# Performance work log

Hardware: AMD Instinct MI355X
Metric: run time of the kernel (lower is better)

## Reference

```python
import jax, jax.numpy as jnp
import numpy as np

D_MODEL = 512
NHEAD = 8
HEAD_DIM = D_MODEL // NHEAD
LN_EPS = 1e-5


def layer_norm(x, gamma, beta):
    mu = jnp.mean(x, axis=-1, keepdims=True)
    var = jnp.var(x, axis=-1, keepdims=True)
    return (x - mu) * jax.lax.rsqrt(var + LN_EPS) * gamma + beta


def setup_inputs() -> dict:
    key = jax.random.key(0)
    ks = jax.random.split(key, 10)
    B, L, S = 2, 4096, 4096
    d = D_MODEL
    s = 0.02
    return {
        "x": jax.random.normal(ks[0], (B, L, d), dtype=jnp.float32),
        "source": jax.random.normal(ks[1], (B, S, d), dtype=jnp.float32),
        "Wq": jax.random.normal(ks[2], (d, d), dtype=jnp.float32) * s,
        "Wk": jax.random.normal(ks[3], (d, d), dtype=jnp.float32) * s,
        "Wv": jax.random.normal(ks[4], (d, d), dtype=jnp.float32) * s,
        "Wm": jax.random.normal(ks[5], (d, d), dtype=jnp.float32) * s,
        "W1": jax.random.normal(ks[6], (2 * d, 2 * d), dtype=jnp.float32) * s,
        "W2": jax.random.normal(ks[7], (d, 2 * d), dtype=jnp.float32) * s,
        "g1": jnp.ones((d,), dtype=jnp.float32),
        "b1": jnp.zeros((d,), dtype=jnp.float32),
        "g2": jnp.ones((d,), dtype=jnp.float32),
        "b2": jnp.zeros((d,), dtype=jnp.float32),
    }


def reference(x, source, Wq, Wk, Wv, Wm, W1, W2, g1, b1, g2, b2):
    bs, L, _ = x.shape
    S = source.shape[1]
    # projections (torch Linear: y = x @ W^T), split into heads
    qw = (x @ Wq.T).reshape(bs, L, NHEAD, HEAD_DIM)
    kw = (source @ Wk.T).reshape(bs, S, NHEAD, HEAD_DIM)
    vw = (source @ Wv.T).reshape(bs, S, NHEAD, HEAD_DIM)
    # attention scores [B, L, S, H], softmax over S (axis=2)
    a = jnp.einsum('nlhd,nshd->nlsh', qw, kw) / jnp.sqrt(jnp.float32(HEAD_DIM))
    a = jax.nn.softmax(a, axis=2)
    o = jnp.einsum('nlsh,nshd->nlhd', a, vw).reshape(bs, L, NHEAD * HEAD_DIM)
    message = layer_norm(o @ Wm.T, g1, b1)
    h = jnp.concatenate([x, message], axis=2)  # [B, L, 2D]
    h = jax.nn.relu(h @ W1.T) @ W2.T
    message = layer_norm(h, g2, b2)
    return x + message
```

## Files before the change

### kernel.cpp

```cpp
#include <hip/hip_runtime.h>
#include <stdint.h>

typedef short bh8 __attribute__((ext_vector_type(8)));
typedef float fx4 __attribute__((ext_vector_type(4)));
typedef float fx16 __attribute__((ext_vector_type(16)));
typedef unsigned short u16;
typedef unsigned int u32;
typedef u32 u32x4 __attribute__((ext_vector_type(4)));
typedef u16 us4 __attribute__((ext_vector_type(4)));

#define NHEAD 8
#define HD 64
#define DM 512
#define SEQ 4096
#define ROWS 8192
#define CEXP 0.1803368801111244f

#define MODE_BF16 1
#define MODE_RELU_BF16 2
#define MODE_KV 3

__device__ __forceinline__ u16 f2bf(float f) {
  union { float f; u32 u; } x; x.f = f;
  u32 u = x.u;
  u = u + 0x7fffu + ((u >> 16) & 1u);
  return (u16)(u >> 16);
}
__device__ __forceinline__ float bf2f(u16 h) {
  union { u32 u; float f; } x; x.u = ((u32)h) << 16;
  return x.f;
}
__device__ __forceinline__ void gll16(const void* g, void* l) {
  __builtin_amdgcn_global_load_lds(
      (const __attribute__((address_space(1))) void*)(uintptr_t)g,
      (__attribute__((address_space(3))) void*)(uintptr_t)l,
      16, 0, 0);
}
__device__ __forceinline__ fx4 mfma16(bh8 a, bh8 b, fx4 c) {
  return __builtin_amdgcn_mfma_f32_16x16x32_bf16(a, b, c, 0, 0, 0);
}
__device__ __forceinline__ fx16 mfma32(bh8 a, bh8 b, fx16 c) {
  return __builtin_amdgcn_mfma_f32_32x32x16_bf16(a, b, c, 0, 0, 0);
}
__device__ __forceinline__ u32 cvtpk(float lo, float hi) {
  u32 r; asm("v_cvt_pk_bf16_f32 %0, %1, %2" : "=v"(r) : "v"(lo), "v"(hi));
  return r;
}
__device__ __forceinline__ void pswap(u32& a, u32& b) {
  auto r = __builtin_amdgcn_permlane32_swap(a, b, false, false);
  a = r[0]; b = r[1];
}

__device__ __forceinline__ int fragidx4(int n, int k4, int K) {
  return (((((n >> 4) * (K >> 5) + (k4 >> 5)) << 2) + ((k4 >> 3) & 3)) * 16 + (n & 15)) * 2
         + ((k4 & 7) >> 2);
}

__global__ __launch_bounds__(256) void cvt_all_kernel(
    const float* __restrict__ x, const float* __restrict__ src,
    const float* __restrict__ Wq, const float* __restrict__ Wk,
    const float* __restrict__ Wv, const float* __restrict__ Wm,
    const float* __restrict__ W1, const float* __restrict__ W2,
    u16* __restrict__ xb, u16* __restrict__ sb,
    u16* __restrict__ wqb, u16* __restrict__ wkvb, u16* __restrict__ wmb,
    u16* __restrict__ w1b, u16* __restrict__ w2b) {
  const int NQ = ROWS * DM / 4;
  const int TOT = 2 * NQ + 655360;
  for (int i = blockIdx.x * 256 + threadIdx.x; i < TOT; i += gridDim.x * 256) {
    const float* s; u16* d; int j; int widx = -1;
    if (i < NQ)            { s = x;  d = xb;  j = i; }
    else if (i < 2 * NQ)   { s = src; d = sb; j = i - NQ; }
    else {
      int k = i - 2 * NQ;
      int n, k4, K;
      if (k < 65536)       { s = Wq; d = wqb; j = k;          n = j >> 7; k4 = (j & 127) << 2; K = 512; }
      else if (k < 131072) { s = Wk; d = wkvb; j = k - 65536; n = j >> 7; k4 = (j & 127) << 2; K = 512; }
      else if (k < 196608) { s = Wv; d = wkvb; j = k - 131072; n = (j >> 7) + 512; k4 = (j & 127) << 2; K = 512; }
      else if (k < 262144) { s = Wm; d = wmb; j = k - 196608; n = j >> 7; k4 = (j & 127) << 2; K = 512; }
      else if (k < 524288) { s = W1; d = w1b; j = k - 262144; n = j >> 8; k4 = (j & 255) << 2; K = 1024; }
      else                 { s = W2; d = w2b; j = k - 524288; n = j >> 8; k4 = (j & 255) << 2; K = 1024; }
      widx = fragidx4(n, k4, K);
    }
    float4 v = ((const float4*)s)[j];
    us4 o; o.x = f2bf(v.x); o.y = f2bf(v.y); o.z = f2bf(v.z); o.w = f2bf(v.w);
    ((us4*)d)[widx < 0 ? j : widx] = o;
  }
}

template <int NTW>
__device__ __forceinline__ void gemm_core(
    char* sA, const u16* __restrict__ A, const u16* __restrict__ A2, int strideA,
    const u16* __restrict__ Bw, void* __restrict__ Cp, void* __restrict__ C2p,
    int N, int K, int mode, float scl, int bx, int by) {
  const int tid = threadIdx.x;
  const int w = tid >> 6, l = tid & 63;
  const int fr = l & 15, fg = l >> 4;
  const int row0 = by * 128, col0 = bx * NTW * 32;
  const int wr = (w >> 1) * 64, wc = (w & 1) * NTW * 16;

  fx4 acc[4][NTW];
#pragma unroll
  for (int m = 0; m < 4; m++)
#pragma unroll
    for (int n = 0; n < NTW; n++)
#pragma unroll
      for (int r = 0; r < 4; r++) acc[m][n][r] = 0.f;

  for (int k0 = 0; k0 < K; k0 += 64) {
    const u16* Asrc = (k0 < 512) ? A : A2;
    const int kk = k0 & (strideA - 1);
    __syncthreads();
#pragma unroll
    for (int i = 0; i < 4; i++) {
      int t = i * 256 + tid;
      int r = t >> 3, g = t & 7;
      int gs = g ^ (r & 7);
      gll16(Asrc + (size_t)(row0 + r) * strideA + kk + gs * 8, sA + i * 4096 + w * 1024);
    }
    bh8 bfr[2][NTW];
#pragma unroll
    for (int ks = 0; ks < 2; ks++)
#pragma unroll
      for (int n = 0; n < NTW; n++) {
        const u16* bp = Bw +
            ((((size_t)((col0 + wc) >> 4) + n) * (K >> 5) + (k0 >> 5) + ks) * 4 + fg) * 128 +
            fr * 8;
        bfr[ks][n] = *(const bh8*)bp;
      }
    __syncthreads();
#pragma unroll
    for (int ks = 0; ks < 2; ks++) {
      bh8 af[4];
#pragma unroll
      for (int m = 0; m < 4; m++) {
        int rr = wr + m * 16 + fr;
        af[m] = *(const bh8*)(sA + rr * 128 + ((ks * 64 + fg * 16) ^ ((rr & 7) << 4)));
      }
      __builtin_amdgcn_s_setprio(1);
#pragma unroll
      for (int m = 0; m < 4; m++)
#pragma unroll
        for (int n = 0; n < NTW; n++) acc[m][n] = mfma16(af[m], bfr[ks][n], acc[m][n]);
      __builtin_amdgcn_s_setprio(0);
    }
  }
#pragma unroll
  for (int m = 0; m < 4; m++)
#pragma unroll
    for (int n = 0; n < NTW; n++)
#pragma unroll
      for (int r = 0; r < 4; r++) {
        int row = row0 + wr + m * 16 + fg * 4 + r;
        int col = col0 + wc + n * 16 + fr;
        float v = acc[m][n][r];
        if (mode == MODE_BF16) {
          ((u16*)Cp)[(size_t)row * N + col] = f2bf(v * scl);
        } else if (mode == MODE_RELU_BF16) {
          ((u16*)Cp)[(size_t)row * N + col] = f2bf(v > 0.f ? v : 0.f);
        } else {
          int bb = row >> 12, s = row & 4095;
          if (col < 512) {
            int h = col >> 6, dd = col & 63;
            ((u16*)Cp)[(((size_t)((bb * 8 + h) * 8 + (dd >> 3))) * SEQ + s) * 8 + (dd & 7)] = f2bf(v);
          } else {
            int dd2 = col - 512;
            int h = dd2 >> 6, dd = dd2 & 63;
            ((u16*)C2p)[(((size_t)((bb * 8 + h) * 512 + (s >> 3))) * 64 + dd) * 8 + (s & 7)] = f2bf(v);
          }
        }
      }
}

__global__ __launch_bounds__(256) void qkv_kernel(
    const u16* __restrict__ xb, const u16* __restrict__ sb,
    const u16* __restrict__ wqb, const u16* __restrict__ wkvb,
    u16* __restrict__ Qb, u16* __restrict__ K2, u16* __restrict__ V2) {
  __shared__ __attribute__((aligned(16))) char smem[128 * 128];
  int bid = blockIdx.x;
  if (bid < 256) {
    gemm_core<4>(smem, xb, xb, 512, wqb, Qb, nullptr, 512, 512, MODE_BF16, CEXP,
                 bid & 3, bid >> 2);
  } else {
    int kb = bid - 256;
    gemm_core<4>(smem, sb, sb, 512, wkvb, K2, V2, 1024, 512, MODE_KV, 1.0f,
                 kb & 7, kb >> 3);
  }
}

__global__ __launch_bounds__(256) void ffn1_kernel(
    const u16* __restrict__ xb, const u16* __restrict__ m0ln,
    const u16* __restrict__ w1b, u16* __restrict__ h1) {
  __shared__ __attribute__((aligned(16))) char smem[128 * 128];
  gemm_core<4>(smem, xb, m0ln, 512, w1b, h1, nullptr, 1024, 1024, MODE_RELU_BF16, 1.0f,
               blockIdx.x, blockIdx.y);
}

__global__ __launch_bounds__(256) void gemm64_kernel(
    const u16* __restrict__ A, const u16* __restrict__ A2, int strideA,
    const u16* __restrict__ Bw, u16* __restrict__ Cp, int K, float scl) {
  __shared__ __attribute__((aligned(16))) char smem[128 * 128];
  gemm_core<2>(smem, A, A2, strideA, Bw, Cp, nullptr, 512, K, MODE_BF16, scl,
               blockIdx.x, blockIdx.y);
}

__global__ __launch_bounds__(256, 3) void attn_kernel(
    const u16* __restrict__ Q, const u16* __restrict__ K2,
    const u16* __restrict__ V2,
    u16* __restrict__ Op0, u16* __restrict__ Op1,
    u16* __restrict__ Op2, u16* __restrict__ Op3,
    float* __restrict__ lsum, int ss) {
  const int tid = threadIdx.x;
  const int w = tid >> 6, l = tid & 63;
  const int l31 = l & 31, hi = l >> 5;

  int dl = blockIdx.x;
  int c = dl & 7, j = dl >> 3;
  int bh = 2 * c + (j >> (5 + ss));
  int rest = j & ((32 << ss) - 1);
  int qb = rest & 31, half = rest >> 5;
  const int b = bh >> 3, h = bh & 7;
  const int qr0 = b * SEQ + qb * 128 + w * 32;
  const int chunk = SEQ >> ss;
  const int sbase = half * chunk;
  const int NT = chunk / 64;

  bh8 qf[4];
#pragma unroll
  for (int ks = 0; ks < 4; ks++)
    qf[ks] = *(const bh8*)(Q + (size_t)(qr0 + l31) * DM + h * HD + ks * 16 + hi * 8);

  const u16* Kbase = K2 + (size_t)bh * 8 * SEQ * 8;
  const u16* Vbase = V2 + (size_t)bh * 512 * 64 * 8;

  fx16 o0, o1;
#pragma unroll
  for (int r = 0; r < 16; r++) { o0[r] = 0.f; o1[r] = 0.f; }
  float l_run = 0.f;

  for (int t = 0; t < NT; ++t) {
    const int s0 = sbase + t * 64;

    bh8 kf0[4], kf1[4];
#pragma unroll
    for (int ks = 0; ks < 4; ks++) {
      const u16* kp = Kbase + ((size_t)(ks * 2 + hi) * SEQ + s0 + l31) * 8;
      kf0[ks] = *(const bh8*)kp;
      kf1[ks] = *(const bh8*)(kp + 32 * 8);
    }

    fx16 s0v, s1v;
#pragma unroll
    for (int r = 0; r < 16; r++) { s0v[r] = 0.f; s1v[r] = 0.f; }
    __builtin_amdgcn_s_setprio(1);
#pragma unroll
    for (int ks = 0; ks < 4; ks++) {
      s0v = mfma32(kf0[ks], qf[ks], s0v);
      s1v = mfma32(kf1[ks], qf[ks], s1v);
    }
    __builtin_amdgcn_s_setprio(0);

    bh8 vf0[4], vf1[4];
#pragma unroll
    for (int ks = 0; ks < 4; ks++) {
      const u16* vp = Vbase + ((size_t)((s0 >> 3) + ks * 2 + hi) * 64 + l31) * 8;
      vf0[ks] = *(const bh8*)vp;
      vf1[ks] = *(const bh8*)(vp + 32 * 8);
    }

    float rs = 0.f;
#pragma unroll
    for (int r = 0; r < 16; r++) {
      s0v[r] = __builtin_amdgcn_exp2f(s0v[r]); rs += s0v[r];
    }
#pragma unroll
    for (int r = 0; r < 16; r++) {
      s1v[r] = __builtin_amdgcn_exp2f(s1v[r]); rs += s1v[r];
    }
    l_run += rs;

    __builtin_amdgcn_s_setprio(1);
#pragma unroll
    for (int ks = 0; ks < 4; ks++) {
      int o8 = (ks & 1) * 8;
      u32 w0a, w1a, w0b, w1b;
      if (ks < 2) {
        w0a = cvtpk(s0v[o8 + 0], s0v[o8 + 1]);
        w1a = cvtpk(s0v[o8 + 2], s0v[o8 + 3]);
        w0b = cvtpk(s0v[o8 + 4], s0v[o8 + 5]);
        w1b = cvtpk(s0v[o8 + 6], s0v[o8 + 7]);
      } else {
        w0a = cvtpk(s1v[o8 + 0], s1v[o8 + 1]);
        w1a = cvtpk(s1v[o8 + 2], s1v[o8 + 3]);
        w0b = cvtpk(s1v[o8 + 4], s1v[o8 + 5]);
        w1b = cvtpk(s1v[o8 + 6], s1v[o8 + 7]);
      }
      pswap(w0a, w0b); pswap(w1a, w1b);
      u32x4 fw; fw.x = w0a; fw.y = w1a; fw.z = w0b; fw.w = w1b;
      bh8 pa = __builtin_bit_cast(bh8, fw);
      o0 = mfma32(pa, vf0[ks], o0);
      o1 = mfma32(pa, vf1[ks], o1);
    }
    __builtin_amdgcn_s_setprio(0);
  }

  l_run += __shfl_xor(l_run, 32);
  if (hi == 0)
    lsum[half * 65536 + bh * 4096 + ((qr0 & 4095) + l31)] = l_run;
  u16* Op = (half == 0) ? Op0 : (half == 1) ? Op1 : (half == 2) ? Op2 : Op3;
#pragma unroll
  for (int r = 0; r < 16; r++) {
    int crow = (r & 3) + 8 * (r >> 2) + 4 * hi;
    size_t row = (size_t)(qr0 + crow);
    Op[row * DM + h * HD + l31] = f2bf(o0[r]);
    Op[row * DM + h * HD + 32 + l31] = f2bf(o1[r]);
  }
}

__global__ __launch_bounds__(256) void merge_kernel(
    const u16* __restrict__ Oa, const u16* __restrict__ Ob,
    const u16* __restrict__ Oc, const u16* __restrict__ Od,
    const float* __restrict__ lsum, u16* __restrict__ out, int split) {
  int i8 = blockIdx.x * 256 + threadIdx.x;
  size_t base = (size_t)i8 * 8;
  if (base >= (size_t)ROWS * DM) return;
  int row = (int)(base >> 9), col = (int)(base & 511);
  int h = col >> 6, b = row >> 12, lr = row & 4095;
  int li = (b * 8 + h) * 4096 + lr;
  float acc[8];
#pragma unroll
  for (int j = 0; j < 8; j++) acc[j] = 0.f;
  float lt = 0.f;
  const u16* ops[4] = {Oa, Ob, Oc, Od};
  for (int s = 0; s < split; s++) {
    lt += lsum[s * 65536 + li];
    bh8 v = *(const bh8*)(ops[s] + base);
#pragma unroll
    for (int j = 0; j < 8; j++) acc[j] += bf2f((u16)v[j]);
  }
  float inv = 1.f / lt;
  bh8 o;
#pragma unroll
  for (int j = 0; j < 8; j++) o[j] = (short)f2bf(acc[j] * inv);
  *(bh8*)(out + base) = o;
}

__global__ __launch_bounds__(256) void ln_kernel(
    const u16* __restrict__ M0, const float* __restrict__ g1,
    const float* __restrict__ b1, u16* __restrict__ out) {
  const int row = blockIdx.x;
  const int tid = threadIdx.x;
  const u16* mr = M0 + (size_t)row * 512;
  float v0 = bf2f(mr[tid]), v1 = bf2f(mr[tid + 256]);
  float s = v0 + v1, s2 = v0 * v0 + v1 * v1;
#pragma unroll
  for (int off = 1; off <= 32; off <<= 1) {
    s += __shfl_xor(s, off);
    s2 += __shfl_xor(s2, off);
  }
  __shared__ float red[8];
  const int w = tid >> 6, l = tid & 63;
  if (l == 0) { red[w] = s; red[w + 4] = s2; }
  __syncthreads();
  s = red[0] + red[1] + red[2] + red[3];
  s2 = red[4] + red[5] + red[6] + red[7];
  float mu = s * (1.f / 512.f);
  float var = s2 * (1.f / 512.f) - mu * mu;
  float rstd = rsqrtf(var + 1e-5f);
  u16* orow = out + (size_t)row * 512;
  for (int e = tid; e < 512; e += 256)
    orow[e] = f2bf((bf2f(mr[e]) - mu) * rstd * g1[e] + b1[e]);
}

__global__ __launch_bounds__(256) void ln_res_kernel(
    const u16* __restrict__ F, const float* __restrict__ X,
    const float* __restrict__ g2, const float* __restrict__ b2,
    float* __restrict__ out) {
  const int row = blockIdx.x;
  const int tid = threadIdx.x;
  const u16* fr_ = F + (size_t)row * 512;
  float v0 = bf2f(fr_[tid]), v1 = bf2f(fr_[tid + 256]);
  float s = v0 + v1, s2 = v0 * v0 + v1 * v1;
#pragma unroll
  for (int off = 1; off <= 32; off <<= 1) {
    s += __shfl_xor(s, off);
    s2 += __shfl_xor(s2, off);
  }
  __shared__ float red[8];
  const int w = tid >> 6, l = tid & 63;
  if (l == 0) { red[w] = s; red[w + 4] = s2; }
  __syncthreads();
  s = red[0] + red[1] + red[2] + red[3];
  s2 = red[4] + red[5] + red[6] + red[7];
  float mu = s * (1.f / 512.f);
  float var = s2 * (1.f / 512.f) - mu * mu;
  float rstd = rsqrtf(var + 1e-5f);
  const float* xr = X + (size_t)row * 512;
  float* orow = out + (size_t)row * 512;
  for (int e = tid; e < 512; e += 256)
    orow[e] = xr[e] + (bf2f(fr_[e]) - mu) * rstd * g2[e] + b2[e];
}

extern "C" void kernel_launch(void* const* d_in, const int* in_sizes, int n_in,
                              void* d_out, int out_size, void* d_ws, size_t ws_size,
                              hipStream_t stream) {
  (void)in_sizes; (void)n_in; (void)out_size;
  const float* x   = (const float*)d_in[0];
  const float* src = (const float*)d_in[1];
  const float* Wq  = (const float*)d_in[2];
  const float* Wk  = (const float*)d_in[3];
  const float* Wv  = (const float*)d_in[4];
  const float* Wm  = (const float*)d_in[5];
  const float* W1  = (const float*)d_in[6];
  const float* W2  = (const float*)d_in[7];
  const float* g1  = (const float*)d_in[8];
  const float* b1  = (const float*)d_in[9];
  const float* g2  = (const float*)d_in[10];
  const float* b2  = (const float*)d_in[11];

  char* ws = (char*)d_ws;
  u16* xb   = (u16*)(ws + 0);
  u16* sb   = (u16*)(ws + 8388608);
  u16* wqb  = (u16*)(ws + 16777216);
  u16* wkvb = (u16*)(ws + 17301504);
  u16* wmb  = (u16*)(ws + 18350080);
  u16* w1b  = (u16*)(ws + 18874368);
  u16* w2b  = (u16*)(ws + 20971520);
  u16* Qb   = (u16*)(ws + 22020096);
  u16* K2b  = (u16*)(ws + 30408704);
  u16* V2b  = (u16*)(ws + 38797312);
  u16* Op0  = (u16*)(ws + 47185920);
  u16* Op1  = (u16*)(ws + 8388608);

  const bool big = ws_size >= 73400320u;
  int ss = big ? 2 : 1;
  u16* Op2; u16* Op3; float* lsum;
  if (big) {
    Op2  = (u16*)(ws + 55574528);
    Op3  = (u16*)(ws + 63963136);
    lsum = (float*)(ws + 72351744);
  } else {
    Op2  = Op0; Op3 = Op0;
    lsum = (float*)(ws + 55574528);
  }
  u16* Obf  = (u16*)(ws + 22020096);
  u16* M0b  = (u16*)(ws + 30408704);
  u16* m0ln = (u16*)(ws + 38797312);
  u16* h1b  = (u16*)(ws + 22020096);
  u16* fb   = (u16*)(ws + 47185920);

  cvt_all_kernel<<<2048, 256, 0, stream>>>(x, src, Wq, Wk, Wv, Wm, W1, W2,
                                           xb, sb, wqb, wkvb, wmb, w1b, w2b);
  qkv_kernel<<<768, 256, 0, stream>>>(xb, sb, wqb, wkvb, Qb, K2b, V2b);
  attn_kernel<<<512 << ss, 256, 0, stream>>>(Qb, K2b, V2b, Op0, Op1, Op2, Op3, lsum, ss);
  merge_kernel<<<2048, 256, 0, stream>>>(Op0, Op1, Op2, Op3, lsum, Obf, 1 << ss);
  gemm64_kernel<<<dim3(8, 64), 256, 0, stream>>>(Obf, Obf, 512, wmb, M0b, 512, 1.0f);
  ln_kernel<<<8192, 256, 0, stream>>>(M0b, g1, b1, m0ln);
  ffn1_kernel<<<dim3(8, 64), 256, 0, stream>>>(xb, m0ln, w1b, h1b);
  gemm64_kernel<<<dim3(8, 64), 256, 0, stream>>>(h1b, h1b, 1024, w2b, fb, 1024, 1.0f);
  ln_res_kernel<<<8192, 256, 0, stream>>>(fb, x, g2, b2, (float*)d_out);
}
```

Baseline: 221.3 us.

## Double-buffer GEMM LDS tiles, strength-reduce attention pointers, fix attention split to two

The shared GEMM core now double-buffers the A tile in LDS, issuing the next tile's global-to-LDS loads before computing the current one and using a single barrier per k-step. The attention kernel precomputes K/V fragment pointers and advances them each tile rather than recomputing addresses. The host always uses a two-way split of the key sequence instead of four-way when workspace allows, reducing merge work but halving the attention grid. Doubling LDS per GEMM block may reduce occupancy.

```diff
diff --git a/kernel.cpp b/kernel.cpp
--- a/kernel.cpp
+++ b/kernel.cpp
@@ -89,7 +89,7 @@
 
 template <int NTW>
 __device__ __forceinline__ void gemm_core(
-    char* sA, const u16* __restrict__ A, const u16* __restrict__ A2, int strideA,
+    char* smem, const u16* __restrict__ A, const u16* __restrict__ A2, int strideA,
     const u16* __restrict__ Bw, void* __restrict__ Cp, void* __restrict__ C2p,
     int N, int K, int mode, float scl, int bx, int by) {
   const int tid = threadIdx.x;
@@ -98,25 +98,33 @@
   const int row0 = by * 128, col0 = bx * NTW * 32;
   const int wr = (w >> 1) * 64, wc = (w & 1) * NTW * 16;
 
-  fx4 acc[4][NTW];
-#pragma unroll
-  for (int m = 0; m < 4; m++)
-#pragma unroll
-    for (int n = 0; n < NTW; n++)
-#pragma unroll
-      for (int r = 0; r < 4; r++) acc[m][n][r] = 0.f;
-
-  for (int k0 = 0; k0 < K; k0 += 64) {
+  auto STAGE = [&](int buf, int k0) {
     const u16* Asrc = (k0 < 512) ? A : A2;
     const int kk = k0 & (strideA - 1);
-    __syncthreads();
+    char* dst = smem + buf * 16384;
 #pragma unroll
     for (int i = 0; i < 4; i++) {
       int t = i * 256 + tid;
-      int r = t >> 3, g = t & 7;
-      int gs = g ^ (r & 7);
-      gll16(Asrc + (size_t)(row0 + r) * strideA + kk + gs * 8, sA + i * 4096 + w * 1024);
-    }
+      int rr = t >> 3, g = t & 7;
+      int gs = g ^ (rr & 7);
+      gll16(Asrc + (size_t)(row0 + rr) * strideA + kk + gs * 8, dst + i * 4096 + w * 1024);
+    }
+  };
+
+  fx4 acc[4][NTW];
+#pragma unroll
+  for (int m = 0; m < 4; m++)
+#pragma unroll
+    for (int n = 0; n < NTW; n++)
+#pragma unroll
+      for (int r = 0; r < 4; r++) acc[m][n][r] = 0.f;
+
+  STAGE(0, 0);
+  __syncthreads();
+
+  const int nk = K / 64;
+  for (int ti = 0; ti < nk; ti++) {
+    const int k0 = ti * 64;
     bh8 bfr[2][NTW];
 #pragma unroll
     for (int ks = 0; ks < 2; ks++)
@@ -127,7 +135,8 @@
             fr * 8;
         bfr[ks][n] = *(const bh8*)bp;
       }
-    __syncthreads();
+    if (ti + 1 < nk) STAGE((ti + 1) & 1, k0 + 64);
+    const char* sA = smem + (ti & 1) * 16384;
 #pragma unroll
     for (int ks = 0; ks < 2; ks++) {
       bh8 af[4];
@@ -143,6 +152,7 @@
         for (int n = 0; n < NTW; n++) acc[m][n] = mfma16(af[m], bfr[ks][n], acc[m][n]);
       __builtin_amdgcn_s_setprio(0);
     }
+    __syncthreads();
   }
 #pragma unroll
   for (int m = 0; m < 4; m++)
@@ -175,7 +185,7 @@
     const u16* __restrict__ xb, const u16* __restrict__ sb,
     const u16* __restrict__ wqb, const u16* __restrict__ wkvb,
     u16* __restrict__ Qb, u16* __restrict__ K2, u16* __restrict__ V2) {
-  __shared__ __attribute__((aligned(16))) char smem[128 * 128];
+  __shared__ __attribute__((aligned(16))) char smem[2 * 16384];
   int bid = blockIdx.x;
   if (bid < 256) {
     gemm_core<4>(smem, xb, xb, 512, wqb, Qb, nullptr, 512, 512, MODE_BF16, CEXP,
@@ -190,7 +200,7 @@
 __global__ __launch_bounds__(256) void ffn1_kernel(
     const u16* __restrict__ xb, const u16* __restrict__ m0ln,
     const u16* __restrict__ w1b, u16* __restrict__ h1) {
-  __shared__ __attribute__((aligned(16))) char smem[128 * 128];
+  __shared__ __attribute__((aligned(16))) char smem[2 * 16384];
   gemm_core<4>(smem, xb, m0ln, 512, w1b, h1, nullptr, 1024, 1024, MODE_RELU_BF16, 1.0f,
                blockIdx.x, blockIdx.y);
 }
@@ -198,7 +208,7 @@
 __global__ __launch_bounds__(256) void gemm64_kernel(
     const u16* __restrict__ A, const u16* __restrict__ A2, int strideA,
     const u16* __restrict__ Bw, u16* __restrict__ Cp, int K, float scl) {
-  __shared__ __attribute__((aligned(16))) char smem[128 * 128];
+  __shared__ __attribute__((aligned(16))) char smem[2 * 16384];
   gemm_core<2>(smem, A, A2, strideA, Bw, Cp, nullptr, 512, K, MODE_BF16, scl,
                blockIdx.x, blockIdx.y);
 }
@@ -232,20 +242,24 @@
   const u16* Kbase = K2 + (size_t)bh * 8 * SEQ * 8;
   const u16* Vbase = V2 + (size_t)bh * 512 * 64 * 8;
 
+  const u16* kp[4]; const u16* vp[4];
+#pragma unroll
+  for (int ks = 0; ks < 4; ks++) {
+    kp[ks] = Kbase + ((size_t)(ks * 2 + hi) * SEQ + sbase + l31) * 8;
+    vp[ks] = Vbase + ((size_t)(((sbase >> 3) + ks * 2 + hi)) * 64 + l31) * 8;
+  }
+
   fx16 o0, o1;
 #pragma unroll
   for (int r = 0; r < 16; r++) { o0[r] = 0.f; o1[r] = 0.f; }
   float l_run = 0.f;
 
   for (int t = 0; t < NT; ++t) {
-    const int s0 = sbase + t * 64;
-
     bh8 kf0[4], kf1[4];
 #pragma unroll
     for (int ks = 0; ks < 4; ks++) {
-      const u16* kp = Kbase + ((size_t)(ks * 2 + hi) * SEQ + s0 + l31) * 8;
-      kf0[ks] = *(const bh8*)kp;
-      kf1[ks] = *(const bh8*)(kp + 32 * 8);
+      kf0[ks] = *(const bh8*)kp[ks];
+      kf1[ks] = *(const bh8*)(kp[ks] + 256);
     }
 
     fx16 s0v, s1v;
@@ -262,10 +276,11 @@
     bh8 vf0[4], vf1[4];
 #pragma unroll
     for (int ks = 0; ks < 4; ks++) {
-      const u16* vp = Vbase + ((size_t)((s0 >> 3) + ks * 2 + hi) * 64 + l31) * 8;
-      vf0[ks] = *(const bh8*)vp;
-      vf1[ks] = *(const bh8*)(vp + 32 * 8);
-    }
+      vf0[ks] = *(const bh8*)vp[ks];
+      vf1[ks] = *(const bh8*)(vp[ks] + 256);
+    }
+#pragma unroll
+    for (int ks = 0; ks < 4; ks++) { kp[ks] += 512; vp[ks] += 4096; }
 
     float rs = 0.f;
 #pragma unroll
@@ -403,7 +418,7 @@
 extern "C" void kernel_launch(void* const* d_in, const int* in_sizes, int n_in,
                               void* d_out, int out_size, void* d_ws, size_t ws_size,
                               hipStream_t stream) {
-  (void)in_sizes; (void)n_in; (void)out_size;
+  (void)in_sizes; (void)n_in; (void)out_size; (void)ws_size;
   const float* x   = (const float*)d_in[0];
   const float* src = (const float*)d_in[1];
   const float* Wq  = (const float*)d_in[2];
@@ -430,18 +445,9 @@
   u16* V2b  = (u16*)(ws + 38797312);
   u16* Op0  = (u16*)(ws + 47185920);
   u16* Op1  = (u16*)(ws + 8388608);
-
-  const bool big = ws_size >= 73400320u;
-  int ss = big ? 2 : 1;
-  u16* Op2; u16* Op3; float* lsum;
-  if (big) {
-    Op2  = (u16*)(ws + 55574528);
-    Op3  = (u16*)(ws + 63963136);
-    lsum = (float*)(ws + 72351744);
-  } else {
-    Op2  = Op0; Op3 = Op0;
-    lsum = (float*)(ws + 55574528);
-  }
+  float* lsum = (float*)(ws + 55574528);
+
+  const int ss = 1;
   u16* Obf  = (u16*)(ws + 22020096);
   u16* M0b  = (u16*)(ws + 30408704);
   u16* m0ln = (u16*)(ws + 38797312);
@@ -451,8 +457,8 @@
   cvt_all_kernel<<<2048, 256, 0, stream>>>(x, src, Wq, Wk, Wv, Wm, W1, W2,
                                            xb, sb, wqb, wkvb, wmb, w1b, w2b);
   qkv_kernel<<<768, 256, 0, stream>>>(xb, sb, wqb, wkvb, Qb, K2b, V2b);
-  attn_kernel<<<512 << ss, 256, 0, stream>>>(Qb, K2b, V2b, Op0, Op1, Op2, Op3, lsum, ss);
-  merge_kernel<<<2048, 256, 0, stream>>>(Op0, Op1, Op2, Op3, lsum, Obf, 1 << ss);
+  attn_kernel<<<512 << ss, 256, 0, stream>>>(Qb, K2b, V2b, Op0, Op1, Op0, Op0, lsum, ss);
+  merge_kernel<<<2048, 256, 0, stream>>>(Op0, Op1, Op0, Op0, lsum, Obf, 1 << ss);
   gemm64_kernel<<<dim3(8, 64), 256, 0, stream>>>(Obf, Obf, 512, wmb, M0b, 512, 1.0f);
   ln_kernel<<<8192, 256, 0, stream>>>(M0b, g1, b1, m0ln);
   ffn1_kernel<<<dim3(8, 64), 256, 0, stream>>>(xb, m0ln, w1b, h1b);
```

Measured after the change: 215.1 us. -2.8%, faster.
